# Performance work log

Measured on AMD Instinct MI355X. Metric: run time of the kernel, lower is better.

The kernel has to match this reference:

```python
import jax, jax.numpy as jnp
import numpy as np

N, E = 100000, 1600000        # nodes, edges
H, D, L = 128, 64, 4          # hidden_size, intermediate_size, num_hidden_layers
ALPHA, THETA = 0.1, 0.5       # GCNII initial-residual / identity-mapping hparams


def setup_inputs() -> dict:
    key = jax.random.key(0)
    ks = jax.random.split(key, 6)
    x = jax.random.normal(ks[0], (N, H), dtype=jnp.float32)
    row = jax.random.randint(ks[1], (E,), 0, N)              # destination nodes
    col = jax.random.randint(ks[2], (E,), 0, N)              # source nodes
    edge_weight = jax.random.uniform(ks[3], (E,), dtype=jnp.float32)
    w_lin = jax.random.normal(ks[4], (H, D), dtype=jnp.float32) / np.sqrt(H)
    b_lin = jnp.zeros((D,), dtype=jnp.float32)
    conv_w = jax.random.normal(ks[5], (L, D, D), dtype=jnp.float32) / np.sqrt(D)
    return {"x": x, "row": row, "col": col, "edge_weight": edge_weight,
            "w_lin": w_lin, "b_lin": b_lin, "conv_w": conv_w}


def reference(x, row, col, edge_weight, w_lin, b_lin, conv_w):
    # Inference mode: dropout layers are identity.
    h = jax.nn.relu(x @ w_lin + b_lin)      # [N, D]
    x0 = h                                   # initial residual
    for l in range(L):
        # GCN2Conv, normalize=False, shared_weights=True, layer index l+1
        beta = jnp.log(THETA / (l + 1) + 1.0).astype(h.dtype)
        msg = h[col] * edge_weight[:, None]                     # [E, D] gather
        agg = jax.ops.segment_sum(msg, row, num_segments=N)     # SpMM: A @ h
        z = (1.0 - ALPHA) * agg + ALPHA * x0                    # residual mix
        h = jax.nn.relu((1.0 - beta) * z + beta * (z @ conv_w[l]))
    return h
```

## Files before the change

kernel.cpp:

```cpp
#include <hip/hip_runtime.h>
#include <hip/hip_fp16.h>
#include <math.h>


#define DD 64
#define HH 128
#define M_TILE 128
#define K_CHUNK 32
#define NPB 128
#define SLOT 2560
#define NBUK_MAX 1024
#define PART_BLOCKS 256
#define PART_THREADS 1024
#define GSTRIDE 17

__device__ inline ushort f2h(float f) { return __half_as_ushort(__float2half(f)); }
__device__ inline float us2f(ushort u) { return __half2float(__ushort_as_half(u)); }

__global__ __launch_bounds__(256) void init_bcur(int* bcur, int nbuk) {
    int i = blockIdx.x * blockDim.x + threadIdx.x;
    if (i < nbuk) bcur[i] = i * SLOT;
}

__global__ __launch_bounds__(PART_THREADS) void partition_kernel(
    const int* __restrict__ row, const int* __restrict__ col,
    const float* __restrict__ ew, int* __restrict__ bcur,
    uint2* __restrict__ pk, int E, int nbuk) {
    __shared__ int cnt[NBUK_MAX], base[NBUK_MAX], rc[NBUK_MAX];
    int t = threadIdx.x;
    for (int i = t; i < nbuk; i += PART_THREADS) { cnt[i] = 0; rc[i] = 0; }
    __syncthreads();
    int chunk = (E + gridDim.x - 1) / gridDim.x;
    int s0 = blockIdx.x * chunk;
    int s1 = min(s0 + chunk, E);
    for (int e = s0 + t; e < s1; e += PART_THREADS)
        atomicAdd(&cnt[__builtin_nontemporal_load(&row[e]) >> 7], 1);
    __syncthreads();
    for (int i = t; i < nbuk; i += PART_THREADS)
        if (cnt[i] > 0) base[i] = atomicAdd(&bcur[i], cnt[i]);
    __syncthreads();
    for (int e = s0 + t; e < s1; e += PART_THREADS) {
        int r = __builtin_nontemporal_load(&row[e]);
        int c = __builtin_nontemporal_load(&col[e]);
        ushort wh = f2h(__builtin_nontemporal_load(&ew[e]));
        int b = r >> 7;
        int pos = base[b] + atomicAdd(&rc[b], 1);
        if (pos < (b + 1) * SLOT)
            pk[pos] = make_uint2((uint)r | (((uint)c & 0x7fffu) << 17),
                                 ((uint)c >> 15) | ((uint)wh << 2));
    }
}

__global__ __launch_bounds__(256) void sort_kernel(
    const uint2* __restrict__ pk, const int* __restrict__ bcur,
    int2* __restrict__ cw, int2* __restrict__ rowptr2, int n) {
    __shared__ int hist[NPB], scan[NPB], rc[NPB];
    int b = blockIdx.x, lo = b << 7;
    int cnt = min(bcur[b] - b * SLOT, SLOT);
    const uint2* rec = pk + (size_t)b * SLOT;
    int t = threadIdx.x;
    if (t < NPB) { hist[t] = 0; rc[t] = 0; }
    __syncthreads();
    for (int i = t; i < cnt; i += 256)
        atomicAdd(&hist[(rec[i].x & 0x1ffffu) - lo], 1);
    __syncthreads();
    if (t < NPB) scan[t] = hist[t];
    __syncthreads();
    for (int off = 1; off < NPB; off <<= 1) {
        int v = (t < NPB && t >= off) ? scan[t - off] : 0;
        __syncthreads();
        if (t < NPB) scan[t] += v;
        __syncthreads();
    }
    if (t < NPB && lo + t < n) {
        int beg = b * SLOT + scan[t] - hist[t];
        rowptr2[lo + t] = make_int2(beg, beg + hist[t]);
    }
    for (int i = t; i < cnt; i += 256) {
        uint2 r2 = rec[i];
        int nl = (int)(r2.x & 0x1ffffu) - lo;
        int c = (int)((r2.x >> 17) | ((r2.y & 3u) << 15));
        float w = us2f((ushort)((r2.y >> 2) & 0xffffu));
        int pos = (scan[nl] - hist[nl]) + atomicAdd(&rc[nl], 1);
        cw[b * SLOT + pos] = make_int2(c, __float_as_int(w));
    }
}

__global__ __launch_bounds__(256) void prep_w(const float* __restrict__ conv_w,
                                              float* __restrict__ Wp, int total) {
    int i = blockIdx.x * blockDim.x + threadIdx.x;
    if (i >= total) return;
    int l = i >> 12;
    int r = i & 4095;
    int d = r >> 6, j = r & 63;
    float beta = logf(0.5f / (float)(l + 1) + 1.0f);
    float v = beta * conv_w[i];
    if (d == j) v += 1.0f - beta;
    Wp[i] = v;
}

__global__ __launch_bounds__(256) void lin0_kernel(
    const float* __restrict__ x, const float* __restrict__ Wlin,
    const float* __restrict__ b, ushort* __restrict__ x0, int n) {
    __shared__ float xs[K_CHUNK][M_TILE];
    int t = threadIdx.x;
    int tm = t >> 4, tn = t & 15;
    int m0 = blockIdx.x * M_TILE;

    float4 bb = *(const float4*)&b[tn * 4];
    float acc[8][4];
#pragma unroll
    for (int mi = 0; mi < 8; ++mi) {
        acc[mi][0] = bb.x; acc[mi][1] = bb.y; acc[mi][2] = bb.z; acc[mi][3] = bb.w;
    }

    float4 v[4];
#pragma unroll
    for (int i = 0; i < 4; ++i) {
        int s = t + i * 256;
        int node = s >> 3, cpos = (s & 7) * 4;
        int g = m0 + node;
        v[i] = (g < n) ? *(const float4*)&x[(size_t)g * HH + cpos]
                       : make_float4(0.f, 0.f, 0.f, 0.f);
    }

    for (int kk = 0; kk < HH; kk += K_CHUNK) {
        __syncthreads();
#pragma unroll
        for (int i = 0; i < 4; ++i) {
            int s = t + i * 256;
            int node = s >> 3, cpos = (s & 7) * 4;
            int q = (s & 7) & 3;
            int pc = node ^ (q << 3);
            xs[cpos + 0][pc] = v[i].x;
            xs[cpos + 1][pc] = v[i].y;
            xs[cpos + 2][pc] = v[i].z;
            xs[cpos + 3][pc] = v[i].w;
        }
        __syncthreads();
        if (kk + K_CHUNK < HH) {
#pragma unroll
            for (int i = 0; i < 4; ++i) {
                int s = t + i * 256;
                int node = s >> 3, cpos = (s & 7) * 4;
                int g = m0 + node;
                v[i] = (g < n)
                    ? *(const float4*)&x[(size_t)g * HH + kk + K_CHUNK + cpos]
                    : make_float4(0.f, 0.f, 0.f, 0.f);
            }
        }
#pragma unroll
        for (int k = 0; k < K_CHUNK; ++k) {
            float4 wv = *(const float4*)&Wlin[(size_t)(kk + k) * DD + tn * 4];
            int base = (tm * 8) ^ ((((k) >> 2) & 3) << 3);
            float4 xa = *(const float4*)&xs[k][base];
            float4 xb = *(const float4*)&xs[k][base + 4];
            float xm[8] = {xa.x, xa.y, xa.z, xa.w, xb.x, xb.y, xb.z, xb.w};
            float wj[4] = {wv.x, wv.y, wv.z, wv.w};
#pragma unroll
            for (int mi = 0; mi < 8; ++mi)
#pragma unroll
                for (int j = 0; j < 4; ++j)
                    acc[mi][j] += xm[mi] * wj[j];
        }
    }
#pragma unroll
    for (int mi = 0; mi < 8; ++mi) {
        int node = m0 + tm * 8 + mi;
        if (node >= n) continue;
        ushort4 o;
        o.x = f2h(fmaxf(acc[mi][0], 0.f));
        o.y = f2h(fmaxf(acc[mi][1], 0.f));
        o.z = f2h(fmaxf(acc[mi][2], 0.f));
        o.w = f2h(fmaxf(acc[mi][3], 0.f));
        *(ushort4*)&x0[(size_t)node * DD + tn * 4] = o;
    }
}

__global__ __launch_bounds__(256) void gather_kernel(
    const ushort* __restrict__ h_in, const ushort* __restrict__ x0,
    const int2* __restrict__ rowptr2, const int2* __restrict__ cw,
    ushort* __restrict__ z, int n) {
    __shared__ int2 es[4][8 * GSTRIDE];
    int wave = threadIdx.x >> 6, lane = threadIdx.x & 63;
    int grp = lane >> 3, sub = lane & 7;
    int2* slot = &es[wave][grp * GSTRIDE];

    int node = (blockIdx.x * 4 + wave) * 8 + grp;
    bool nvalid = node < n;
    int nn = nvalid ? node : (n - 1);
    int2 rp = rowptr2[nn];
    int beg = rp.x;
    int end = nvalid ? rp.y : beg;
    uint4 x0v = *(const uint4*)&x0[(size_t)nn * DD + sub * 8];

    float acc[4][8];
#pragma unroll
    for (int c = 0; c < 4; ++c)
#pragma unroll
        for (int f = 0; f < 8; ++f) acc[c][f] = 0.f;

    for (int base = beg; base < end; base += 16) {
        int m = end - base;
        if (m > 16) m = 16;
        if (sub < m) slot[sub] = cw[base + sub];
        if (sub + 8 < m) slot[sub + 8] = cw[base + sub + 8];
#pragma unroll
        for (int j = 0; j < 4; ++j) {
#pragma unroll
            for (int c = 0; c < 4; ++c) {
                int idx = j * 4 + c;
                bool vld = idx < m;
                int2 r = slot[vld ? idx : 0];
                float w = vld ? __int_as_float(r.y) : 0.f;
                uint4 hv = *(const uint4*)&h_in[(size_t)r.x * DD + sub * 8];
                acc[c][0] += w * us2f((ushort)(hv.x & 0xffff));
                acc[c][1] += w * us2f((ushort)(hv.x >> 16));
                acc[c][2] += w * us2f((ushort)(hv.y & 0xffff));
                acc[c][3] += w * us2f((ushort)(hv.y >> 16));
                acc[c][4] += w * us2f((ushort)(hv.z & 0xffff));
                acc[c][5] += w * us2f((ushort)(hv.z >> 16));
                acc[c][6] += w * us2f((ushort)(hv.w & 0xffff));
                acc[c][7] += w * us2f((ushort)(hv.w >> 16));
            }
        }
    }
    if (nvalid) {
        float f[8];
#pragma unroll
        for (int k = 0; k < 8; ++k)
            f[k] = (acc[0][k] + acc[1][k]) + (acc[2][k] + acc[3][k]);
        uint xp[4] = {x0v.x, x0v.y, x0v.z, x0v.w};
        uint o[4];
#pragma unroll
        for (int p = 0; p < 4; ++p) {
            float zlo = 0.9f * f[2 * p]     + 0.1f * us2f((ushort)(xp[p] & 0xffff));
            float zhi = 0.9f * f[2 * p + 1] + 0.1f * us2f((ushort)(xp[p] >> 16));
            o[p] = (uint)f2h(zlo) | ((uint)f2h(zhi) << 16);
        }
        *(uint4*)&z[(size_t)node * DD + sub * 8] =
            make_uint4(o[0], o[1], o[2], o[3]);
    }
}

__global__ __launch_bounds__(256) void dense_kernel(
    const ushort* __restrict__ zin, const float* __restrict__ Wp,
    ushort* __restrict__ h_half, float* __restrict__ h_f32, int n) {
    __shared__ float xs[K_CHUNK][M_TILE];
    int t = threadIdx.x;
    int tm = t >> 4, tn = t & 15;
    int m0 = blockIdx.x * M_TILE;

    float acc[8][4];
#pragma unroll
    for (int mi = 0; mi < 8; ++mi)
#pragma unroll
        for (int j = 0; j < 4; ++j) acc[mi][j] = 0.f;

    for (int kk = 0; kk < DD; kk += K_CHUNK) {
        __syncthreads();
#pragma unroll
        for (int i = 0; i < 4; ++i) {
            int s = t + i * 256;
            int node = s >> 3;
            int cpos = (s & 7) * 4;
            int g = m0 + node;
            ushort4 v = make_ushort4(0, 0, 0, 0);
            if (g < n) v = *(const ushort4*)&zin[(size_t)g * DD + kk + cpos];
            int q = (s & 7) & 3;
            int pc = node ^ (q << 3);
            xs[cpos + 0][pc] = us2f(v.x);
            xs[cpos + 1][pc] = us2f(v.y);
            xs[cpos + 2][pc] = us2f(v.z);
            xs[cpos + 3][pc] = us2f(v.w);
        }
        __syncthreads();
#pragma unroll
        for (int k = 0; k < K_CHUNK; ++k) {
            float4 wv = *(const float4*)&Wp[(size_t)(kk + k) * DD + tn * 4];
            int base = (tm * 8) ^ (((k >> 2) & 3) << 3);
            float4 xa = *(const float4*)&xs[k][base];
            float4 xb = *(const float4*)&xs[k][base + 4];
            float xm[8] = {xa.x, xa.y, xa.z, xa.w, xb.x, xb.y, xb.z, xb.w};
            float wj[4] = {wv.x, wv.y, wv.z, wv.w};
#pragma unroll
            for (int mi = 0; mi < 8; ++mi)
#pragma unroll
                for (int j = 0; j < 4; ++j)
                    acc[mi][j] += xm[mi] * wj[j];
        }
    }
#pragma unroll
    for (int mi = 0; mi < 8; ++mi) {
        int node = m0 + tm * 8 + mi;
        if (node >= n) continue;
        float o0 = fmaxf(acc[mi][0], 0.f);
        float o1 = fmaxf(acc[mi][1], 0.f);
        float o2 = fmaxf(acc[mi][2], 0.f);
        float o3 = fmaxf(acc[mi][3], 0.f);
        if (h_f32) {
            *(float4*)&h_f32[(size_t)node * DD + tn * 4] =
                make_float4(o0, o1, o2, o3);
        } else {
            ushort4 o;
            o.x = f2h(o0); o.y = f2h(o1); o.z = f2h(o2); o.w = f2h(o3);
            *(ushort4*)&h_half[(size_t)node * DD + tn * 4] = o;
        }
    }
}

static inline size_t align256(size_t x) { return (x + 255) & ~(size_t)255; }

extern "C" void kernel_launch(void* const* d_in, const int* in_sizes, int n_in,
                              void* d_out, int out_size, void* d_ws, size_t ws_size,
                              hipStream_t stream) {
    const float* x      = (const float*)d_in[0];
    const int*   row    = (const int*)d_in[1];
    const int*   col    = (const int*)d_in[2];
    const float* ew     = (const float*)d_in[3];
    const float* w_lin  = (const float*)d_in[4];
    const float* b_lin  = (const float*)d_in[5];
    const float* conv_w = (const float*)d_in[6];
    float* out = (float*)d_out;

    const int N = in_sizes[0] / HH;
    const int E = in_sizes[1];
    const int L = in_sizes[6] / (DD * DD);
    const int nbuk = (N + NPB - 1) / NPB;

    char* ws = (char*)d_ws;
    size_t off = 0;
    int* bcur = (int*)(ws + off);        off = align256(off + (size_t)NBUK_MAX * 4);
    uint2* pk = (uint2*)(ws + off);      off = align256(off + (size_t)nbuk * SLOT * 8);
    int2* cw = (int2*)(ws + off);        off = align256(off + (size_t)nbuk * SLOT * 8);
    int2* rowptr2 = (int2*)(ws + off);   off = align256(off + (size_t)N * 8);
    ushort* x0 = (ushort*)(ws + off);    off = align256(off + (size_t)N * DD * 2);
    ushort* hA = (ushort*)(ws + off);    off = align256(off + (size_t)N * DD * 2);
    ushort* hB = (ushort*)(ws + off);    off = align256(off + (size_t)N * DD * 2);
    ushort* zb = (ushort*)(ws + off);    off = align256(off + (size_t)N * DD * 2);
    float* Wp = (float*)(ws + off);      off = align256(off + (size_t)L * DD * DD * 4);
    (void)ws_size;

    const int mt = (N + M_TILE - 1) / M_TILE;
    const int gb = (N + 31) / 32;

    init_bcur<<<(nbuk + 255) / 256, 256, 0, stream>>>(bcur, nbuk);
    partition_kernel<<<PART_BLOCKS, PART_THREADS, 0, stream>>>(row, col, ew, bcur, pk, E, nbuk);
    sort_kernel<<<nbuk, 256, 0, stream>>>(pk, bcur, cw, rowptr2, N);

    int total = L * DD * DD;
    prep_w<<<(total + 255) / 256, 256, 0, stream>>>(conv_w, Wp, total);

    lin0_kernel<<<mt, 256, 0, stream>>>(x, w_lin, b_lin, x0, N);

    for (int l = 0; l < L; ++l) {
        const ushort* hin = (l == 0) ? x0 : ((l % 2 == 1) ? hB : hA);
        ushort* hout      = (l % 2 == 0) ? hB : hA;
        gather_kernel<<<gb, 256, 0, stream>>>(hin, x0, rowptr2, cw, zb, N);
        bool last = (l == L - 1);
        dense_kernel<<<mt, 256, 0, stream>>>(zb, Wp + (size_t)l * DD * DD,
                                             last ? nullptr : hout,
                                             last ? out : nullptr, N);
    }
}
```

Measured before the change: 305.3 us.

## Fuse SpMM gather and dense GEMM into a single per-layer kernel

Merges the gather/aggregate kernel and the dense 64x64 matmul kernel into one layer kernel. The aggregated z rows for 32 nodes stay in shared memory as fp32 and are multiplied by a shared-memory copy of the layer weight. This removes the fp16 z round trip through global memory and one launch per layer. In exchange, every block reloads the 16KB weight tile, uses more LDS, and adds a block-wide sync between the gather and GEMM phases, which may lower occupancy.

```diff
diff --git a/kernel.cpp b/kernel.cpp
--- a/kernel.cpp
+++ b/kernel.cpp
@@ -13,6 +13,7 @@
 #define PART_BLOCKS 256
 #define PART_THREADS 1024
 #define GSTRIDE 17
+#define WPAD 68
 
 __device__ inline ushort f2h(float f) { return __half_as_ushort(__float2half(f)); }
 __device__ inline float us2f(ushort u) { return __half2float(__ushort_as_half(u)); }
@@ -177,16 +178,29 @@
     }
 }
 
-__global__ __launch_bounds__(256) void gather_kernel(
+__global__ __launch_bounds__(256) void layer_kernel(
     const ushort* __restrict__ h_in, const ushort* __restrict__ x0,
     const int2* __restrict__ rowptr2, const int2* __restrict__ cw,
-    ushort* __restrict__ z, int n) {
+    const float* __restrict__ Wp, ushort* __restrict__ h_half,
+    float* __restrict__ h_f32, int n) {
+    __shared__ float Ws[DD][WPAD];
+    __shared__ float zs[32][WPAD];
     __shared__ int2 es[4][8 * GSTRIDE];
-    int wave = threadIdx.x >> 6, lane = threadIdx.x & 63;
+    int t = threadIdx.x;
+
+    {
+        int k = t >> 2, j0 = (t & 3) * 16;
+#pragma unroll
+        for (int p = 0; p < 4; ++p)
+            *(float4*)&Ws[k][j0 + p * 4] =
+                *(const float4*)&Wp[(size_t)k * DD + j0 + p * 4];
+    }
+
+    int wave = t >> 6, lane = t & 63;
     int grp = lane >> 3, sub = lane & 7;
     int2* slot = &es[wave][grp * GSTRIDE];
-
-    int node = (blockIdx.x * 4 + wave) * 8 + grp;
+    int ln = wave * 8 + grp;
+    int node = blockIdx.x * 32 + ln;
     bool nvalid = node < n;
     int nn = nvalid ? node : (n - 1);
     int2 rp = rowptr2[nn];
@@ -225,86 +239,52 @@
             }
         }
     }
-    if (nvalid) {
-        float f[8];
-#pragma unroll
-        for (int k = 0; k < 8; ++k)
-            f[k] = (acc[0][k] + acc[1][k]) + (acc[2][k] + acc[3][k]);
+    {
         uint xp[4] = {x0v.x, x0v.y, x0v.z, x0v.w};
-        uint o[4];
-#pragma unroll
-        for (int p = 0; p < 4; ++p) {
-            float zlo = 0.9f * f[2 * p]     + 0.1f * us2f((ushort)(xp[p] & 0xffff));
-            float zhi = 0.9f * f[2 * p + 1] + 0.1f * us2f((ushort)(xp[p] >> 16));
-            o[p] = (uint)f2h(zlo) | ((uint)f2h(zhi) << 16);
-        }
-        *(uint4*)&z[(size_t)node * DD + sub * 8] =
-            make_uint4(o[0], o[1], o[2], o[3]);
-    }
-}
-
-__global__ __launch_bounds__(256) void dense_kernel(
-    const ushort* __restrict__ zin, const float* __restrict__ Wp,
-    ushort* __restrict__ h_half, float* __restrict__ h_f32, int n) {
-    __shared__ float xs[K_CHUNK][M_TILE];
-    int t = threadIdx.x;
-    int tm = t >> 4, tn = t & 15;
-    int m0 = blockIdx.x * M_TILE;
-
-    float acc[8][4];
-#pragma unroll
-    for (int mi = 0; mi < 8; ++mi)
-#pragma unroll
-        for (int j = 0; j < 4; ++j) acc[mi][j] = 0.f;
-
-    for (int kk = 0; kk < DD; kk += K_CHUNK) {
-        __syncthreads();
-#pragma unroll
-        for (int i = 0; i < 4; ++i) {
-            int s = t + i * 256;
-            int node = s >> 3;
-            int cpos = (s & 7) * 4;
-            int g = m0 + node;
-            ushort4 v = make_ushort4(0, 0, 0, 0);
-            if (g < n) v = *(const ushort4*)&zin[(size_t)g * DD + kk + cpos];
-            int q = (s & 7) & 3;
-            int pc = node ^ (q << 3);
-            xs[cpos + 0][pc] = us2f(v.x);
-            xs[cpos + 1][pc] = us2f(v.y);
-            xs[cpos + 2][pc] = us2f(v.z);
-            xs[cpos + 3][pc] = us2f(v.w);
-        }
-        __syncthreads();
-#pragma unroll
-        for (int k = 0; k < K_CHUNK; ++k) {
-            float4 wv = *(const float4*)&Wp[(size_t)(kk + k) * DD + tn * 4];
-            int base = (tm * 8) ^ (((k >> 2) & 3) << 3);
-            float4 xa = *(const float4*)&xs[k][base];
-            float4 xb = *(const float4*)&xs[k][base + 4];
-            float xm[8] = {xa.x, xa.y, xa.z, xa.w, xb.x, xb.y, xb.z, xb.w};
-            float wj[4] = {wv.x, wv.y, wv.z, wv.w};
-#pragma unroll
-            for (int mi = 0; mi < 8; ++mi)
-#pragma unroll
-                for (int j = 0; j < 4; ++j)
-                    acc[mi][j] += xm[mi] * wj[j];
-        }
-    }
-#pragma unroll
-    for (int mi = 0; mi < 8; ++mi) {
-        int node = m0 + tm * 8 + mi;
-        if (node >= n) continue;
-        float o0 = fmaxf(acc[mi][0], 0.f);
-        float o1 = fmaxf(acc[mi][1], 0.f);
-        float o2 = fmaxf(acc[mi][2], 0.f);
-        float o3 = fmaxf(acc[mi][3], 0.f);
+        float4 za, zb2;
+        float* zo[2] = {&za.x, &zb2.x};
+#pragma unroll
+        for (int k = 0; k < 8; ++k) {
+            float f = (acc[0][k] + acc[1][k]) + (acc[2][k] + acc[3][k]);
+            float xv = (k & 1) ? us2f((ushort)(xp[k >> 1] >> 16))
+                               : us2f((ushort)(xp[k >> 1] & 0xffff));
+            zo[k >> 2][k & 3] = 0.9f * f + 0.1f * xv;
+        }
+        *(float4*)&zs[ln][sub * 8] = za;
+        *(float4*)&zs[ln][sub * 8 + 4] = zb2;
+    }
+    __syncthreads();
+
+    int ln2 = t >> 3, tn = t & 7;
+    int gnode = blockIdx.x * 32 + ln2;
+    float o[8];
+#pragma unroll
+    for (int j = 0; j < 8; ++j) o[j] = 0.f;
+#pragma unroll
+    for (int k = 0; k < DD; ++k) {
+        float zk = zs[ln2][k];
+        float4 wa = *(const float4*)&Ws[k][tn * 8];
+        float4 wb = *(const float4*)&Ws[k][tn * 8 + 4];
+        o[0] += zk * wa.x; o[1] += zk * wa.y;
+        o[2] += zk * wa.z; o[3] += zk * wa.w;
+        o[4] += zk * wb.x; o[5] += zk * wb.y;
+        o[6] += zk * wb.z; o[7] += zk * wb.w;
+    }
+    if (gnode < n) {
+#pragma unroll
+        for (int j = 0; j < 8; ++j) o[j] = fmaxf(o[j], 0.f);
         if (h_f32) {
-            *(float4*)&h_f32[(size_t)node * DD + tn * 4] =
-                make_float4(o0, o1, o2, o3);
+            *(float4*)&h_f32[(size_t)gnode * DD + tn * 8] =
+                make_float4(o[0], o[1], o[2], o[3]);
+            *(float4*)&h_f32[(size_t)gnode * DD + tn * 8 + 4] =
+                make_float4(o[4], o[5], o[6], o[7]);
         } else {
-            ushort4 o;
-            o.x = f2h(o0); o.y = f2h(o1); o.z = f2h(o2); o.w = f2h(o3);
-            *(ushort4*)&h_half[(size_t)node * DD + tn * 4] = o;
+            uint4 ov;
+            ov.x = (uint)f2h(o[0]) | ((uint)f2h(o[1]) << 16);
+            ov.y = (uint)f2h(o[2]) | ((uint)f2h(o[3]) << 16);
+            ov.z = (uint)f2h(o[4]) | ((uint)f2h(o[5]) << 16);
+            ov.w = (uint)f2h(o[6]) | ((uint)f2h(o[7]) << 16);
+            *(uint4*)&h_half[(size_t)gnode * DD + tn * 8] = ov;
         }
     }
 }
@@ -337,7 +317,6 @@
     ushort* x0 = (ushort*)(ws + off);    off = align256(off + (size_t)N * DD * 2);
     ushort* hA = (ushort*)(ws + off);    off = align256(off + (size_t)N * DD * 2);
     ushort* hB = (ushort*)(ws + off);    off = align256(off + (size_t)N * DD * 2);
-    ushort* zb = (ushort*)(ws + off);    off = align256(off + (size_t)N * DD * 2);
     float* Wp = (float*)(ws + off);      off = align256(off + (size_t)L * DD * DD * 4);
     (void)ws_size;
 
@@ -356,9 +335,9 @@
     for (int l = 0; l < L; ++l) {
         const ushort* hin = (l == 0) ? x0 : ((l % 2 == 1) ? hB : hA);
         ushort* hout      = (l % 2 == 0) ? hB : hA;
-        gather_kernel<<<gb, 256, 0, stream>>>(hin, x0, rowptr2, cw, zb, N);
         bool last = (l == L - 1);
-        dense_kernel<<<mt, 256, 0, stream>>>(zb, Wp + (size_t)l * DD * DD,
+        layer_kernel<<<gb, 256, 0, stream>>>(hin, x0, rowptr2, cw,
+                                             Wp + (size_t)l * DD * DD,
                                              last ? nullptr : hout,
                                              last ? out : nullptr, N);
     }
```

New measurement: 299.9 us (median of 2 runs). About the same (-1.8%).
